# Kernel optimization log

Hardware: AMD Instinct MI355X
Metric: run time of the kernel (lower is better)

Reference implementation:

```python
import jax, jax.numpy as jnp
import numpy as np
from jax import lax

B, T, E, H, VC, VP = 128, 512, 256, 512, 64, 128


def _uniform(key, shape, bound):
    return jax.random.uniform(key, shape, minval=-bound, maxval=bound, dtype=jnp.float32)


def setup_inputs() -> dict:
    key = jax.random.key(0)
    ks = jax.random.split(key, 12)
    src = jax.random.randint(ks[0], (B, T), 0, VC)
    src_lengths = jax.random.randint(ks[1], (B,), 1, T + 1)
    # embedding table, padding_idx=0 row zeroed (as nn.Embedding does)
    emb_table = jax.random.normal(ks[2], (VC, E), dtype=jnp.float32)
    emb_table = emb_table.at[0].set(0.0)
    # layer 0: W_xh Linear(E->H, bias), W_hh Linear(H->H, no bias)
    bE, bH = 1.0 / np.sqrt(E), 1.0 / np.sqrt(H)
    W_xh0 = _uniform(ks[3], (E, H), bE)
    b_xh0 = _uniform(ks[4], (H,), bE)
    W_hh0 = _uniform(ks[5], (H, H), bH)
    # layer 1: input is hidden of layer 0
    W_xh1 = _uniform(ks[6], (H, H), bH)
    b_xh1 = _uniform(ks[7], (H,), bH)
    W_hh1 = _uniform(ks[8], (H, H), bH)
    # output projection Linear(H -> VP)
    fc_w = _uniform(ks[9], (H, VP), bH)
    fc_b = _uniform(ks[10], (VP,), bH)
    return {
        "src": src, "src_lengths": src_lengths, "emb_table": emb_table,
        "W_xh0": W_xh0, "b_xh0": b_xh0, "W_hh0": W_hh0,
        "W_xh1": W_xh1, "b_xh1": b_xh1, "W_hh1": W_hh1,
        "fc_w": fc_w, "fc_b": fc_b,
    }


def reference(src, src_lengths, emb_table, W_xh0, b_xh0, W_hh0,
              W_xh1, b_xh1, W_hh1, fc_w, fc_b):
    batch, seq_len = src.shape
    emb = emb_table[src]  # (B, T, E); dropout p=0 -> identity (eval)
    mask = jnp.arange(seq_len)[None, :] < src_lengths[:, None]  # (B, T) bool

    xs = jnp.transpose(emb, (1, 0, 2))          # (T, B, E) time-major
    ms = jnp.transpose(mask)[:, :, None]        # (T, B, 1)

    def step(h, inp):
        x_t, m_t = inp
        h0, h1 = h
        h0_new = jnp.tanh(x_t @ W_xh0 + b_xh0 + h0 @ W_hh0)
        h0 = jnp.where(m_t, h0_new, h0)
        h1_new = jnp.tanh(h0 @ W_xh1 + b_xh1 + h1 @ W_hh1)
        h1 = jnp.where(m_t, h1_new, h1)
        return (h0, h1), h1

    h_init = jnp.zeros((batch, W_hh0.shape[0]), dtype=emb.dtype)
    _, ys = lax.scan(step, (h_init, h_init), (xs, ms))  # ys: (T, B, H)
    outputs = jnp.transpose(ys, (1, 0, 2))               # (B, T, H)
    logits = outputs @ fc_w + fc_b                       # (B, T, VP)
    return logits
```

## Files before the change

### kernel.cpp

```cpp
#include <hip/hip_runtime.h>
#include <hip/hip_bf16.h>

constexpr int NB = 128;
constexpr int NT = 512;
constexpr int NE = 256;
constexpr int NH = 512;
constexpr int NV = 64;
constexpr int NP = 128;

constexpr int GROUPS = 8;
constexpr int MR     = 16;
constexpr int NCS    = 64;
constexpr int SLICES = 8;
constexpr int NBLK   = GROUPS * SLICES;
constexpr int RING   = 16;
constexpr int FS     = 32;

typedef unsigned short u16;
typedef __attribute__((ext_vector_type(8))) short bf16x8v;
typedef __attribute__((ext_vector_type(4))) float f32x4v;
typedef __attribute__((ext_vector_type(4))) unsigned u32x4;

__device__ __forceinline__ u16 f2bf(float x) {
  unsigned u = __builtin_bit_cast(unsigned, x);
  return (u16)((u + 0x7fffu + ((u >> 16) & 1u)) >> 16);
}

__device__ __forceinline__ void ld2_sc1_x4(const void* p0, const void* p1,
                                           u32x4& a, u32x4& b) {
  asm volatile("global_load_dwordx4 %0, %2, off sc1\n\t"
               "global_load_dwordx4 %1, %3, off sc1\n\t"
               "s_waitcnt vmcnt(0)"
               : "=&v"(a), "=&v"(b) : "v"(p0), "v"(p1) : "memory");
}
__device__ __forceinline__ void ld4_sc1_x4(const void* p0, const void* p1,
                                           const void* p2, const void* p3,
                                           u32x4& a, u32x4& b,
                                           u32x4& c, u32x4& d) {
  asm volatile("global_load_dwordx4 %0, %4, off sc1\n\t"
               "global_load_dwordx4 %1, %5, off sc1\n\t"
               "global_load_dwordx4 %2, %6, off sc1\n\t"
               "global_load_dwordx4 %3, %7, off sc1\n\t"
               "s_waitcnt vmcnt(0)"
               : "=&v"(a), "=&v"(b), "=&v"(c), "=&v"(d)
               : "v"(p0), "v"(p1), "v"(p2), "v"(p3) : "memory");
}
__device__ __forceinline__ void st_sc1_x4(void* p, u32x4 v) {
  asm volatile("global_store_dwordx4 %0, %1, off sc1" :: "v"(p), "v"(v) : "memory");
}

__global__ __launch_bounds__(256) void proj_kernel(
    const float* __restrict__ emb, const float* __restrict__ W_xh0,
    const float* __restrict__ b_xh0, float* __restrict__ proj) {
  int v = blockIdx.x >> 1;
  int j = ((blockIdx.x & 1) << 8) + threadIdx.x;
  float acc = b_xh0[j];
  const float* er = emb + v * NE;
  for (int e = 0; e < NE; ++e) acc += er[e] * W_xh0[e * NH + j];
  proj[v * NH + j] = acc;
}

__global__ __launch_bounds__(256) void transpose_bf16_kernel(
    const float* __restrict__ src, u16* __restrict__ dst, int R, int logC) {
  int idx = blockIdx.x * 256 + threadIdx.x;
  int C = 1 << logC;
  if (idx >= R * C) return;
  int r = idx >> logC;
  int c = idx & (C - 1);
  dst[c * R + r] = f2bf(src[idx]);
}

__global__ void zero_flags_kernel(int* flags) {
  int i = blockIdx.x * 256 + threadIdx.x;
  if (i < NBLK * FS) flags[i] = 0;
}

__device__ __forceinline__ bf16x8v frag_A(const u16* __restrict__ buf,
                                          int kt, int lane) {
  return *(const bf16x8v*)(buf + (kt << 9) + (((lane ^ kt) & 63) << 3));
}

__global__ __launch_bounds__(512, 1) void rnn_persist(
    const int* __restrict__ src, const int* __restrict__ lens,
    const float* __restrict__ proj,
    const u16* __restrict__ Wt_hh0,
    const u16* __restrict__ Wt_xh1,
    const u16* __restrict__ Wt_hh1,
    const float* __restrict__ b_xh1,
    u16* __restrict__ h0_ring,
    u16* __restrict__ h1_all,
    int* __restrict__ flags)
{
  __shared__ struct {
    u16 a0[16 * 512];
    u16 a1[16 * 512];
    float pj[NV][72];
    int srcv[MR][NT];
    u16 rep0[16][72];
    u16 rep1[16][72];
  } sm;

  const int bid = blockIdx.x;
  const int g = bid & (GROUPS - 1);
  const int slice = bid >> 3;
  const int c0 = slice * NCS;
  const int r0 = g * MR;

  const int tid = threadIdx.x;
  const int lane = tid & 63, wave = tid >> 6;
  const int lq = lane >> 4, lr = lane & 15;
  const bool l1w = (wave >= 4);
  const int n0 = (wave & 3) * 16;
  const size_t HS = (size_t)NB * NH;

  int* myflag = flags + bid * FS;

  bf16x8v w0[16], wx[16], wh[16];
  if (!l1w) {
    const u16* wp = Wt_hh0 + (size_t)(c0 + n0 + lr) * NH + lq * 8;
#pragma unroll
    for (int kt = 0; kt < 16; ++kt) w0[kt] = *(const bf16x8v*)(wp + kt * 32);
  } else {
    const u16* wpx = Wt_xh1 + (size_t)(c0 + n0 + lr) * NH + lq * 8;
    const u16* wph = Wt_hh1 + (size_t)(c0 + n0 + lr) * NH + lq * 8;
#pragma unroll
    for (int kt = 0; kt < 16; ++kt) {
      wx[kt] = *(const bf16x8v*)(wpx + kt * 32);
      wh[kt] = *(const bf16x8v*)(wph + kt * 32);
    }
  }
  const float bcol = l1w ? b_xh1[c0 + n0 + lr] : 0.f;

#pragma unroll
  for (int it = 0; it < 2; ++it) {
    int c = it * 512 + tid;
    int v = c >> 4, j4 = (c & 15) * 4;
    *(float4*)&sm.pj[v][j4] = *(const float4*)&proj[v * NH + c0 + j4];
  }
#pragma unroll
  for (int it = 0; it < 4; ++it)
    ((int4*)sm.srcv)[it * 512 + tid] =
        ((const int4*)(src + (size_t)r0 * NT))[it * 512 + tid];

  int ln[4];
#pragma unroll
  for (int i = 0; i < 4; ++i) ln[i] = lens[r0 + lq * 4 + i];
  u16 oreg[4] = {0, 0, 0, 0};
  __syncthreads();

  for (int s = 0; s <= NT; ++s) {
    if (s > 0) {
      if (tid < 8) {
        const int* fp = flags + (((tid * 8) | g)) * FS;
        while (__hip_atomic_load(fp, __ATOMIC_RELAXED,
                                 __HIP_MEMORY_SCOPE_AGENT) < s) {}
      }
      if (tid < 64) __builtin_amdgcn_fence(__ATOMIC_ACQUIRE, "agent");
      __syncthreads();
      {
        const u16* g0 = h0_ring + (size_t)((s - 1) & (RING - 1)) * HS +
                        (size_t)r0 * NH;
        int idx0 = tid, idx1 = 512 + tid;
        int row0 = idx0 >> 6, k80 = idx0 & 63;
        int row1 = idx1 >> 6, k81 = idx1 & 63;
        int kt0 = k80 >> 2, s0 = (((k80 & 3) << 4) | row0) ^ kt0;
        int kt1 = k81 >> 2, s1 = (((k81 & 3) << 4) | row1) ^ kt1;
        if (s >= 2) {
          const u16* g1 = h1_all + (size_t)(s - 2) * HS + (size_t)r0 * NH;
          u32x4 a, b, c, d;
          ld4_sc1_x4(g0 + row0 * NH + k80 * 8, g0 + row1 * NH + k81 * 8,
                     g1 + row0 * NH + k80 * 8, g1 + row1 * NH + k81 * 8,
                     a, b, c, d);
          *(u32x4*)(sm.a0 + (kt0 << 9) + (s0 << 3)) = a;
          *(u32x4*)(sm.a0 + (kt1 << 9) + (s1 << 3)) = b;
          *(u32x4*)(sm.a1 + (kt0 << 9) + (s0 << 3)) = c;
          *(u32x4*)(sm.a1 + (kt1 << 9) + (s1 << 3)) = d;
        } else {
          u32x4 a, b;
          ld2_sc1_x4(g0 + row0 * NH + k80 * 8, g0 + row1 * NH + k81 * 8, a, b);
          *(u32x4*)(sm.a0 + (kt0 << 9) + (s0 << 3)) = a;
          *(u32x4*)(sm.a0 + (kt1 << 9) + (s1 << 3)) = b;
        }
      }
      __syncthreads();
    }

    if (!l1w) {
      if (s < NT) {
        f32x4v acc = {0.f, 0.f, 0.f, 0.f};
        if (s > 0) {
#pragma unroll
          for (int kt = 0; kt < 16; ++kt)
            acc = __builtin_amdgcn_mfma_f32_16x16x32_bf16(
                frag_A(sm.a0, kt, lane), w0[kt], acc, 0, 0, 0);
        }
#pragma unroll
        for (int i = 0; i < 4; ++i) {
          int row = lq * 4 + i;
          float pre = acc[i] + sm.pj[sm.srcv[row][s]][n0 + lr];
          oreg[i] = (s < ln[i]) ? f2bf(tanhf(pre)) : oreg[i];
          sm.rep0[row][n0 + lr] = oreg[i];
        }
      }
    } else {
      if (s >= 1) {
        const int t = s - 1;
        f32x4v accx = {0.f, 0.f, 0.f, 0.f}, acch = {0.f, 0.f, 0.f, 0.f};
#pragma unroll
        for (int kt = 0; kt < 16; ++kt)
          accx = __builtin_amdgcn_mfma_f32_16x16x32_bf16(
              frag_A(sm.a0, kt, lane), wx[kt], accx, 0, 0, 0);
        if (s >= 2) {
#pragma unroll
          for (int kt = 0; kt < 16; ++kt)
            acch = __builtin_amdgcn_mfma_f32_16x16x32_bf16(
                frag_A(sm.a1, kt, lane), wh[kt], acch, 0, 0, 0);
        }
#pragma unroll
        for (int i = 0; i < 4; ++i) {
          int row = lq * 4 + i;
          float pre = accx[i] + acch[i] + bcol;
          oreg[i] = (t < ln[i]) ? f2bf(tanhf(pre)) : oreg[i];
          sm.rep1[row][n0 + lr] = oreg[i];
        }
      }
    }
    __syncthreads();

    if (tid < 256) {
      int p = tid >> 7, e = tid & 127;
      int row = e >> 3, q = e & 7;
      if (p == 0) {
        if (s < NT)
          st_sc1_x4(h0_ring + (size_t)(s & (RING - 1)) * HS +
                        (size_t)(r0 + row) * NH + c0 + q * 8,
                    *(const u32x4*)&sm.rep0[row][q * 8]);
      } else if (s >= 1) {
        st_sc1_x4(h1_all + (size_t)(s - 1) * HS +
                      (size_t)(r0 + row) * NH + c0 + q * 8,
                  *(const u32x4*)&sm.rep1[row][q * 8]);
      }
    }
    asm volatile("s_waitcnt vmcnt(0)" ::: "memory");
    __syncthreads();
    if (tid == 0)
      __hip_atomic_store(myflag, s + 1, __ATOMIC_RELAXED,
                         __HIP_MEMORY_SCOPE_AGENT);
  }
}

__global__ __launch_bounds__(256) void out_gemm(
    const u16* __restrict__ h1_all, const u16* __restrict__ fc_wT,
    const float* __restrict__ fc_b, float* __restrict__ out)
{
  const int t = blockIdx.x;
  const int tid = threadIdx.x, lane = tid & 63, wave = tid >> 6;
  const int lq = lane >> 4, lr = lane & 15;
  const int m0 = wave * 32;
  f32x4v acc[2][8];
#pragma unroll
  for (int a = 0; a < 2; ++a)
#pragma unroll
    for (int b = 0; b < 8; ++b) acc[a][b] = (f32x4v){0.f, 0.f, 0.f, 0.f};

  const u16* a0p = h1_all + ((size_t)t * NB + m0 + lr) * NH;
  const u16* a1p = a0p + 16 * NH;
#pragma unroll 2
  for (int kt = 0; kt < 16; ++kt) {
    int kb = kt * 32 + lq * 8;
    bf16x8v a0 = *(const bf16x8v*)(a0p + kb);
    bf16x8v a1 = *(const bf16x8v*)(a1p + kb);
#pragma unroll
    for (int ni = 0; ni < 8; ++ni) {
      bf16x8v bb = *(const bf16x8v*)(fc_wT + (size_t)(ni * 16 + lr) * NH + kb);
      acc[0][ni] = __builtin_amdgcn_mfma_f32_16x16x32_bf16(a0, bb, acc[0][ni], 0, 0, 0);
      acc[1][ni] = __builtin_amdgcn_mfma_f32_16x16x32_bf16(a1, bb, acc[1][ni], 0, 0, 0);
    }
  }
#pragma unroll
  for (int mi = 0; mi < 2; ++mi)
#pragma unroll
    for (int ni = 0; ni < 8; ++ni)
#pragma unroll
      for (int i = 0; i < 4; ++i) {
        int b_ = m0 + mi * 16 + lq * 4 + i;
        int p = ni * 16 + lr;
        out[((size_t)b_ * NT + t) * NP + p] = acc[mi][ni][i] + fc_b[p];
      }
}

extern "C" void kernel_launch(void* const* d_in, const int* in_sizes, int n_in,
                              void* d_out, int out_size, void* d_ws, size_t ws_size,
                              hipStream_t stream) {
  const int*   src   = (const int*)  d_in[0];
  const int*   lens  = (const int*)  d_in[1];
  const float* emb   = (const float*)d_in[2];
  const float* W_xh0 = (const float*)d_in[3];
  const float* b_xh0 = (const float*)d_in[4];
  const float* W_hh0 = (const float*)d_in[5];
  const float* W_xh1 = (const float*)d_in[6];
  const float* b_xh1 = (const float*)d_in[7];
  const float* W_hh1 = (const float*)d_in[8];
  const float* fc_w  = (const float*)d_in[9];
  const float* fc_b  = (const float*)d_in[10];
  float* out = (float*)d_out;

  char* ws = (char*)d_ws;
  auto alloc = [&](size_t bytes) { char* p = ws; ws += (bytes + 255) & ~size_t(255); return p; };
  float* proj   = (float*)alloc(NV * NH * 4);
  u16* Wt_hh0   = (u16*)  alloc(NH * NH * 2);
  u16* Wt_xh1   = (u16*)  alloc(NH * NH * 2);
  u16* Wt_hh1   = (u16*)  alloc(NH * NH * 2);
  u16* fc_wT    = (u16*)  alloc(NP * NH * 2);
  u16* h0_ring  = (u16*)  alloc((size_t)RING * NB * NH * 2);
  u16* h1_all   = (u16*)  alloc((size_t)NT * NB * NH * 2);
  int* flags    = (int*)  alloc(NBLK * FS * 4);

  proj_kernel<<<NV * 2, 256, 0, stream>>>(emb, W_xh0, b_xh0, proj);
  transpose_bf16_kernel<<<(NH * NH + 255) / 256, 256, 0, stream>>>(W_hh0, Wt_hh0, NH, 9);
  transpose_bf16_kernel<<<(NH * NH + 255) / 256, 256, 0, stream>>>(W_xh1, Wt_xh1, NH, 9);
  transpose_bf16_kernel<<<(NH * NH + 255) / 256, 256, 0, stream>>>(W_hh1, Wt_hh1, NH, 9);
  transpose_bf16_kernel<<<(NH * NP + 255) / 256, 256, 0, stream>>>(fc_w, fc_wT, NH, 7);
  zero_flags_kernel<<<(NBLK * FS + 255) / 256, 256, 0, stream>>>(flags);

  {
    void* kargs[] = { (void*)&src, (void*)&lens, (void*)&proj, (void*)&Wt_hh0,
                      (void*)&Wt_xh1, (void*)&Wt_hh1, (void*)&b_xh1,
                      (void*)&h0_ring, (void*)&h1_all, (void*)&flags };
    hipError_t e = hipLaunchCooperativeKernel((void*)rnn_persist, dim3(NBLK), dim3(512),
                                              kargs, 0, stream);
    if (e != hipSuccess) {
      rnn_persist<<<NBLK, 512, 0, stream>>>(src, lens, proj, Wt_hh0, Wt_xh1,
                                            Wt_hh1, b_xh1, h0_ring, h1_all, flags);
    }
  }

  out_gemm<<<NT, 256, 0, stream>>>(h1_all, fc_wT, fc_b, out);
}
```

Before: 1.833 ms.

## Split RNN layers into separate block sets with pre-swizzled fragment layout

Splits the persistent kernel so layer 0 and layer 1 run on separate 256-thread blocks (128 blocks total) with their own flag arrays. Layer 0 can now run up to RING-2 steps ahead of layer 1 instead of advancing in lockstep. Hidden states are published in an MFMA-fragment-swizzled panel layout, so loads copy straight into LDS without per-element index math, and out_gemm reads that layout directly. The cost is twice as many blocks needing co-residency and more cross-block flag polling.

Result: faster. 1.547 ms (-15.6%).

```diff
diff --git a/kernel.cpp b/kernel.cpp
--- a/kernel.cpp
+++ b/kernel.cpp
@@ -12,7 +12,7 @@
 constexpr int MR     = 16;
 constexpr int NCS    = 64;
 constexpr int SLICES = 8;
-constexpr int NBLK   = GROUPS * SLICES;
+constexpr int NBLK   = GROUPS * SLICES * 2;
 constexpr int RING   = 16;
 constexpr int FS     = 32;
 
@@ -26,17 +26,9 @@
   return (u16)((u + 0x7fffu + ((u >> 16) & 1u)) >> 16);
 }
 
-__device__ __forceinline__ void ld2_sc1_x4(const void* p0, const void* p1,
-                                           u32x4& a, u32x4& b) {
-  asm volatile("global_load_dwordx4 %0, %2, off sc1\n\t"
-               "global_load_dwordx4 %1, %3, off sc1\n\t"
-               "s_waitcnt vmcnt(0)"
-               : "=&v"(a), "=&v"(b) : "v"(p0), "v"(p1) : "memory");
-}
-__device__ __forceinline__ void ld4_sc1_x4(const void* p0, const void* p1,
-                                           const void* p2, const void* p3,
-                                           u32x4& a, u32x4& b,
-                                           u32x4& c, u32x4& d) {
+__device__ __forceinline__ void ld4_sc1(const void* p0, const void* p1,
+                                        const void* p2, const void* p3,
+                                        u32x4& a, u32x4& b, u32x4& c, u32x4& d) {
   asm volatile("global_load_dwordx4 %0, %4, off sc1\n\t"
                "global_load_dwordx4 %1, %5, off sc1\n\t"
                "global_load_dwordx4 %2, %6, off sc1\n\t"
@@ -44,6 +36,26 @@
                "s_waitcnt vmcnt(0)"
                : "=&v"(a), "=&v"(b), "=&v"(c), "=&v"(d)
                : "v"(p0), "v"(p1), "v"(p2), "v"(p3) : "memory");
+}
+__device__ __forceinline__ void ld8_sc1(const void* p0, const void* p1,
+                                        const void* p2, const void* p3,
+                                        const void* p4, const void* p5,
+                                        const void* p6, const void* p7,
+                                        u32x4& a, u32x4& b, u32x4& c, u32x4& d,
+                                        u32x4& e, u32x4& f, u32x4& g, u32x4& h) {
+  asm volatile("global_load_dwordx4 %0, %8, off sc1\n\t"
+               "global_load_dwordx4 %1, %9, off sc1\n\t"
+               "global_load_dwordx4 %2, %10, off sc1\n\t"
+               "global_load_dwordx4 %3, %11, off sc1\n\t"
+               "global_load_dwordx4 %4, %12, off sc1\n\t"
+               "global_load_dwordx4 %5, %13, off sc1\n\t"
+               "global_load_dwordx4 %6, %14, off sc1\n\t"
+               "global_load_dwordx4 %7, %15, off sc1\n\t"
+               "s_waitcnt vmcnt(0)"
+               : "=&v"(a), "=&v"(b), "=&v"(c), "=&v"(d),
+                 "=&v"(e), "=&v"(f), "=&v"(g), "=&v"(h)
+               : "v"(p0), "v"(p1), "v"(p2), "v"(p3),
+                 "v"(p4), "v"(p5), "v"(p6), "v"(p7) : "memory");
 }
 __device__ __forceinline__ void st_sc1_x4(void* p, u32x4 v) {
   asm volatile("global_store_dwordx4 %0, %1, off sc1" :: "v"(p), "v"(v) : "memory");
@@ -72,7 +84,7 @@
 
 __global__ void zero_flags_kernel(int* flags) {
   int i = blockIdx.x * 256 + threadIdx.x;
-  if (i < NBLK * FS) flags[i] = 0;
+  if (i < 2 * 64 * FS) flags[i] = 0;
 }
 
 __device__ __forceinline__ bf16x8v frag_A(const u16* __restrict__ buf,
@@ -80,177 +92,218 @@
   return *(const bf16x8v*)(buf + (kt << 9) + (((lane ^ kt) & 63) << 3));
 }
 
-__global__ __launch_bounds__(512, 1) void rnn_persist(
+__device__ __forceinline__ void publish_slice(const u16* __restrict__ rep,
+                                              u16* __restrict__ gpanel,
+                                              int sl, int tid) {
+  if (tid < 128) {
+    int ktl = tid >> 6, slot = tid & 63;
+    int ktp = sl * 2 + ktl;
+    int v = (slot ^ ktp) & 63;
+    int row = v & 15, koct = (v >> 4) & 3;
+    int lcol = ktl * 32 + koct * 8;
+    st_sc1_x4(gpanel + ktp * 512 + slot * 8,
+              *(const u32x4*)(rep + row * 64 + lcol));
+  }
+}
+
+__global__ __launch_bounds__(256, 1) void rnn_persist(
     const int* __restrict__ src, const int* __restrict__ lens,
     const float* __restrict__ proj,
     const u16* __restrict__ Wt_hh0,
     const u16* __restrict__ Wt_xh1,
     const u16* __restrict__ Wt_hh1,
     const float* __restrict__ b_xh1,
-    u16* __restrict__ h0_ring,
-    u16* __restrict__ h1_all,
+    u16* __restrict__ h0f,
+    u16* __restrict__ h1f,
     int* __restrict__ flags)
 {
   __shared__ struct {
-    u16 a0[16 * 512];
-    u16 a1[16 * 512];
-    float pj[NV][72];
-    int srcv[MR][NT];
-    u16 rep0[16][72];
-    u16 rep1[16][72];
+    union {
+      struct { __attribute__((aligned(16))) u16 a0[8192];
+               float pj[NV][68]; int srcv[MR][NT]; } l0;
+      struct { __attribute__((aligned(16))) u16 a0[8192];
+               __attribute__((aligned(16))) u16 a1[8192]; } l1;
+    } u;
+    __attribute__((aligned(16))) u16 rep[16][64];
   } sm;
 
   const int bid = blockIdx.x;
-  const int g = bid & (GROUPS - 1);
-  const int slice = bid >> 3;
-  const int c0 = slice * NCS;
+  const bool is_l1 = (bid >= 64);
+  const int rb = bid & 63;
+  const int g = rb & (GROUPS - 1);
+  const int sl = rb >> 3;
+  const int c0 = sl * NCS;
   const int r0 = g * MR;
 
   const int tid = threadIdx.x;
   const int lane = tid & 63, wave = tid >> 6;
   const int lq = lane >> 4, lr = lane & 15;
-  const bool l1w = (wave >= 4);
-  const int n0 = (wave & 3) * 16;
-  const size_t HS = (size_t)NB * NH;
-
-  int* myflag = flags + bid * FS;
-
-  bf16x8v w0[16], wx[16], wh[16];
-  if (!l1w) {
-    const u16* wp = Wt_hh0 + (size_t)(c0 + n0 + lr) * NH + lq * 8;
-#pragma unroll
-    for (int kt = 0; kt < 16; ++kt) w0[kt] = *(const bf16x8v*)(wp + kt * 32);
-  } else {
-    const u16* wpx = Wt_xh1 + (size_t)(c0 + n0 + lr) * NH + lq * 8;
-    const u16* wph = Wt_hh1 + (size_t)(c0 + n0 + lr) * NH + lq * 8;
-#pragma unroll
-    for (int kt = 0; kt < 16; ++kt) {
-      wx[kt] = *(const bf16x8v*)(wpx + kt * 32);
-      wh[kt] = *(const bf16x8v*)(wph + kt * 32);
-    }
-  }
-  const float bcol = l1w ? b_xh1[c0 + n0 + lr] : 0.f;
-
-#pragma unroll
-  for (int it = 0; it < 2; ++it) {
-    int c = it * 512 + tid;
-    int v = c >> 4, j4 = (c & 15) * 4;
-    *(float4*)&sm.pj[v][j4] = *(const float4*)&proj[v * NH + c0 + j4];
-  }
-#pragma unroll
-  for (int it = 0; it < 4; ++it)
-    ((int4*)sm.srcv)[it * 512 + tid] =
-        ((const int4*)(src + (size_t)r0 * NT))[it * 512 + tid];
+  const int lcol = wave * 16 + lr;
+
+  int* flag0 = flags;
+  int* flag1 = flags + 64 * FS;
+  int* myflag = (is_l1 ? flag1 : flag0) + rb * FS;
 
   int ln[4];
 #pragma unroll
   for (int i = 0; i < 4; ++i) ln[i] = lens[r0 + lq * 4 + i];
   u16 oreg[4] = {0, 0, 0, 0};
-  __syncthreads();
-
-  for (int s = 0; s <= NT; ++s) {
-    if (s > 0) {
+
+  if (!is_l1) {
+    bf16x8v w0[16];
+    {
+      const u16* wp = Wt_hh0 + (size_t)(c0 + lcol) * NH + lq * 8;
+#pragma unroll
+      for (int kt = 0; kt < 16; ++kt) w0[kt] = *(const bf16x8v*)(wp + kt * 32);
+    }
+#pragma unroll
+    for (int it = 0; it < 4; ++it) {
+      int c = it * 256 + tid;
+      int v = c >> 4, j4 = (c & 15) * 4;
+      *(float4*)&sm.u.l0.pj[v][j4] = *(const float4*)&proj[v * NH + c0 + j4];
+    }
+#pragma unroll
+    for (int it = 0; it < 8; ++it)
+      ((int4*)sm.u.l0.srcv)[it * 256 + tid] =
+          ((const int4*)(src + (size_t)r0 * NT))[it * 256 + tid];
+    __syncthreads();
+
+    for (int s = 0; s < NT; ++s) {
+      f32x4v acc = {0.f, 0.f, 0.f, 0.f};
+      if (s > 0) {
+        if (tid < 8) {
+          const int* fp = flag0 + ((tid * 8) | g) * FS;
+          while (__hip_atomic_load(fp, __ATOMIC_RELAXED,
+                                   __HIP_MEMORY_SCOPE_AGENT) < s) {}
+        } else if (tid < 16 && s - 14 > 0) {
+          const int* fp = flag1 + (((tid - 8) * 8) | g) * FS;
+          while (__hip_atomic_load(fp, __ATOMIC_RELAXED,
+                                   __HIP_MEMORY_SCOPE_AGENT) < s - 14) {}
+        }
+        if (tid < 64) __builtin_amdgcn_fence(__ATOMIC_ACQUIRE, "agent");
+        __syncthreads();
+        {
+          const u16* gp = h0f + ((size_t)((s - 1) & (RING - 1)) * GROUPS + g) * 8192;
+          u32x4 a, b, c, d;
+          ld4_sc1(gp + (tid + 0) * 8, gp + (tid + 256) * 8,
+                  gp + (tid + 512) * 8, gp + (tid + 768) * 8, a, b, c, d);
+          *(u32x4*)(sm.u.l0.a0 + (tid + 0) * 8) = a;
+          *(u32x4*)(sm.u.l0.a0 + (tid + 256) * 8) = b;
+          *(u32x4*)(sm.u.l0.a0 + (tid + 512) * 8) = c;
+          *(u32x4*)(sm.u.l0.a0 + (tid + 768) * 8) = d;
+        }
+        __syncthreads();
+#pragma unroll
+        for (int kt = 0; kt < 16; ++kt)
+          acc = __builtin_amdgcn_mfma_f32_16x16x32_bf16(
+              frag_A(sm.u.l0.a0, kt, lane), w0[kt], acc, 0, 0, 0);
+      }
+#pragma unroll
+      for (int i = 0; i < 4; ++i) {
+        int row = lq * 4 + i;
+        float pre = acc[i] + sm.u.l0.pj[sm.u.l0.srcv[row][s]][lcol];
+        oreg[i] = (s < ln[i]) ? f2bf(tanhf(pre)) : oreg[i];
+        sm.rep[row][lcol] = oreg[i];
+      }
+      __syncthreads();
+      publish_slice(&sm.rep[0][0],
+                    h0f + ((size_t)(s & (RING - 1)) * GROUPS + g) * 8192, sl, tid);
+      asm volatile("s_waitcnt vmcnt(0)" ::: "memory");
+      __syncthreads();
+      if (tid == 0)
+        __hip_atomic_store(myflag, s + 1, __ATOMIC_RELAXED,
+                           __HIP_MEMORY_SCOPE_AGENT);
+    }
+  } else {
+    bf16x8v wx[16], wh[16];
+    {
+      const u16* wpx = Wt_xh1 + (size_t)(c0 + lcol) * NH + lq * 8;
+      const u16* wph = Wt_hh1 + (size_t)(c0 + lcol) * NH + lq * 8;
+#pragma unroll
+      for (int kt = 0; kt < 16; ++kt) {
+        wx[kt] = *(const bf16x8v*)(wpx + kt * 32);
+        wh[kt] = *(const bf16x8v*)(wph + kt * 32);
+      }
+    }
+    const float bcol = b_xh1[c0 + lcol];
+    __syncthreads();
+
+    for (int t = 0; t < NT; ++t) {
       if (tid < 8) {
-        const int* fp = flags + (((tid * 8) | g)) * FS;
+        if (t > 0) {
+          const int* fp = flag1 + ((tid * 8) | g) * FS;
+          while (__hip_atomic_load(fp, __ATOMIC_RELAXED,
+                                   __HIP_MEMORY_SCOPE_AGENT) < t) {}
+        }
+      } else if (tid < 16) {
+        const int* fp = flag0 + (((tid - 8) * 8) | g) * FS;
         while (__hip_atomic_load(fp, __ATOMIC_RELAXED,
-                                 __HIP_MEMORY_SCOPE_AGENT) < s) {}
+                                 __HIP_MEMORY_SCOPE_AGENT) < t + 1) {}
       }
       if (tid < 64) __builtin_amdgcn_fence(__ATOMIC_ACQUIRE, "agent");
       __syncthreads();
       {
-        const u16* g0 = h0_ring + (size_t)((s - 1) & (RING - 1)) * HS +
-                        (size_t)r0 * NH;
-        int idx0 = tid, idx1 = 512 + tid;
-        int row0 = idx0 >> 6, k80 = idx0 & 63;
-        int row1 = idx1 >> 6, k81 = idx1 & 63;
-        int kt0 = k80 >> 2, s0 = (((k80 & 3) << 4) | row0) ^ kt0;
-        int kt1 = k81 >> 2, s1 = (((k81 & 3) << 4) | row1) ^ kt1;
-        if (s >= 2) {
-          const u16* g1 = h1_all + (size_t)(s - 2) * HS + (size_t)r0 * NH;
+        const u16* g0 = h0f + ((size_t)(t & (RING - 1)) * GROUPS + g) * 8192;
+        if (t > 0) {
+          const u16* g1 = h1f + ((size_t)(t - 1) * GROUPS + g) * 8192;
+          u32x4 a, b, c, d, e, f, h, k;
+          ld8_sc1(g0 + (tid + 0) * 8, g0 + (tid + 256) * 8,
+                  g0 + (tid + 512) * 8, g0 + (tid + 768) * 8,
+                  g1 + (tid + 0) * 8, g1 + (tid + 256) * 8,
+                  g1 + (tid + 512) * 8, g1 + (tid + 768) * 8,
+                  a, b, c, d, e, f, h, k);
+          *(u32x4*)(sm.u.l1.a0 + (tid + 0) * 8) = a;
+          *(u32x4*)(sm.u.l1.a0 + (tid + 256) * 8) = b;
+          *(u32x4*)(sm.u.l1.a0 + (tid + 512) * 8) = c;
+          *(u32x4*)(sm.u.l1.a0 + (tid + 768) * 8) = d;
+          *(u32x4*)(sm.u.l1.a1 + (tid + 0) * 8) = e;
+          *(u32x4*)(sm.u.l1.a1 + (tid + 256) * 8) = f;
+          *(u32x4*)(sm.u.l1.a1 + (tid + 512) * 8) = h;
+          *(u32x4*)(sm.u.l1.a1 + (tid + 768) * 8) = k;
+        } else {
           u32x4 a, b, c, d;
-          ld4_sc1_x4(g0 + row0 * NH + k80 * 8, g0 + row1 * NH + k81 * 8,
-                     g1 + row0 * NH + k80 * 8, g1 + row1 * NH + k81 * 8,
-                     a, b, c, d);
-          *(u32x4*)(sm.a0 + (kt0 << 9) + (s0 << 3)) = a;
-          *(u32x4*)(sm.a0 + (kt1 << 9) + (s1 << 3)) = b;
-          *(u32x4*)(sm.a1 + (kt0 << 9) + (s0 << 3)) = c;
-          *(u32x4*)(sm.a1 + (kt1 << 9) + (s1 << 3)) = d;
-        } else {
-          u32x4 a, b;
-          ld2_sc1_x4(g0 + row0 * NH + k80 * 8, g0 + row1 * NH + k81 * 8, a, b);
-          *(u32x4*)(sm.a0 + (kt0 << 9) + (s0 << 3)) = a;
-          *(u32x4*)(sm.a0 + (kt1 << 9) + (s1 << 3)) = b;
+          ld4_sc1(g0 + (tid + 0) * 8, g0 + (tid + 256) * 8,
+                  g0 + (tid + 512) * 8, g0 + (tid + 768) * 8, a, b, c, d);
+          *(u32x4*)(sm.u.l1.a0 + (tid + 0) * 8) = a;
+          *(u32x4*)(sm.u.l1.a0 + (tid + 256) * 8) = b;
+          *(u32x4*)(sm.u.l1.a0 + (tid + 512) * 8) = c;
+          *(u32x4*)(sm.u.l1.a0 + (tid + 768) * 8) = d;
         }
       }
       __syncthreads();
-    }
-
-    if (!l1w) {
-      if (s < NT) {
-        f32x4v acc = {0.f, 0.f, 0.f, 0.f};
-        if (s > 0) {
-#pragma unroll
-          for (int kt = 0; kt < 16; ++kt)
-            acc = __builtin_amdgcn_mfma_f32_16x16x32_bf16(
-                frag_A(sm.a0, kt, lane), w0[kt], acc, 0, 0, 0);
-        }
-#pragma unroll
-        for (int i = 0; i < 4; ++i) {
-          int row = lq * 4 + i;
-          float pre = acc[i] + sm.pj[sm.srcv[row][s]][n0 + lr];
-          oreg[i] = (s < ln[i]) ? f2bf(tanhf(pre)) : oreg[i];
-          sm.rep0[row][n0 + lr] = oreg[i];
-        }
-      }
-    } else {
-      if (s >= 1) {
-        const int t = s - 1;
-        f32x4v accx = {0.f, 0.f, 0.f, 0.f}, acch = {0.f, 0.f, 0.f, 0.f};
+
+      f32x4v accx = {0.f, 0.f, 0.f, 0.f}, acch = {0.f, 0.f, 0.f, 0.f};
+#pragma unroll
+      for (int kt = 0; kt < 16; ++kt)
+        accx = __builtin_amdgcn_mfma_f32_16x16x32_bf16(
+            frag_A(sm.u.l1.a0, kt, lane), wx[kt], accx, 0, 0, 0);
+      if (t > 0) {
 #pragma unroll
         for (int kt = 0; kt < 16; ++kt)
-          accx = __builtin_amdgcn_mfma_f32_16x16x32_bf16(
-              frag_A(sm.a0, kt, lane), wx[kt], accx, 0, 0, 0);
-        if (s >= 2) {
-#pragma unroll
-          for (int kt = 0; kt < 16; ++kt)
-            acch = __builtin_amdgcn_mfma_f32_16x16x32_bf16(
-                frag_A(sm.a1, kt, lane), wh[kt], acch, 0, 0, 0);
-        }
-#pragma unroll
-        for (int i = 0; i < 4; ++i) {
-          int row = lq * 4 + i;
-          float pre = accx[i] + acch[i] + bcol;
-          oreg[i] = (t < ln[i]) ? f2bf(tanhf(pre)) : oreg[i];
-          sm.rep1[row][n0 + lr] = oreg[i];
-        }
-      }
-    }
-    __syncthreads();
-
-    if (tid < 256) {
-      int p = tid >> 7, e = tid & 127;
-      int row = e >> 3, q = e & 7;
-      if (p == 0) {
-        if (s < NT)
-          st_sc1_x4(h0_ring + (size_t)(s & (RING - 1)) * HS +
-                        (size_t)(r0 + row) * NH + c0 + q * 8,
-                    *(const u32x4*)&sm.rep0[row][q * 8]);
-      } else if (s >= 1) {
-        st_sc1_x4(h1_all + (size_t)(s - 1) * HS +
-                      (size_t)(r0 + row) * NH + c0 + q * 8,
-                  *(const u32x4*)&sm.rep1[row][q * 8]);
-      }
-    }
-    asm volatile("s_waitcnt vmcnt(0)" ::: "memory");
-    __syncthreads();
-    if (tid == 0)
-      __hip_atomic_store(myflag, s + 1, __ATOMIC_RELAXED,
-                         __HIP_MEMORY_SCOPE_AGENT);
+          acch = __builtin_amdgcn_mfma_f32_16x16x32_bf16(
+              frag_A(sm.u.l1.a1, kt, lane), wh[kt], acch, 0, 0, 0);
+      }
+#pragma unroll
+      for (int i = 0; i < 4; ++i) {
+        int row = lq * 4 + i;
+        float pre = accx[i] + acch[i] + bcol;
+        oreg[i] = (t < ln[i]) ? f2bf(tanhf(pre)) : oreg[i];
+        sm.rep[row][lcol] = oreg[i];
+      }
+      __syncthreads();
+      publish_slice(&sm.rep[0][0],
+                    h1f + ((size_t)t * GROUPS + g) * 8192, sl, tid);
+      asm volatile("s_waitcnt vmcnt(0)" ::: "memory");
+      __syncthreads();
+      if (tid == 0)
+        __hip_atomic_store(myflag, t + 1, __ATOMIC_RELAXED,
+                           __HIP_MEMORY_SCOPE_AGENT);
+    }
   }
 }
 
 __global__ __launch_bounds__(256) void out_gemm(
-    const u16* __restrict__ h1_all, const u16* __restrict__ fc_wT,
+    const u16* __restrict__ h1f, const u16* __restrict__ fc_wT,
     const float* __restrict__ fc_b, float* __restrict__ out)
 {
   const int t = blockIdx.x;
@@ -263,13 +316,13 @@
 #pragma unroll
     for (int b = 0; b < 8; ++b) acc[a][b] = (f32x4v){0.f, 0.f, 0.f, 0.f};
 
-  const u16* a0p = h1_all + ((size_t)t * NB + m0 + lr) * NH;
-  const u16* a1p = a0p + 16 * NH;
+  const u16* p0 = h1f + ((size_t)t * GROUPS + wave * 2) * 8192;
+  const u16* p1 = p0 + 8192;
 #pragma unroll 2
   for (int kt = 0; kt < 16; ++kt) {
+    bf16x8v a0 = *(const bf16x8v*)(p0 + kt * 512 + (((lane ^ kt) & 63) << 3));
+    bf16x8v a1 = *(const bf16x8v*)(p1 + kt * 512 + (((lane ^ kt) & 63) << 3));
     int kb = kt * 32 + lq * 8;
-    bf16x8v a0 = *(const bf16x8v*)(a0p + kb);
-    bf16x8v a1 = *(const bf16x8v*)(a1p + kb);
 #pragma unroll
     for (int ni = 0; ni < 8; ++ni) {
       bf16x8v bb = *(const bf16x8v*)(fc_wT + (size_t)(ni * 16 + lr) * NH + kb);
@@ -312,28 +365,28 @@
   u16* Wt_xh1   = (u16*)  alloc(NH * NH * 2);
   u16* Wt_hh1   = (u16*)  alloc(NH * NH * 2);
   u16* fc_wT    = (u16*)  alloc(NP * NH * 2);
-  u16* h0_ring  = (u16*)  alloc((size_t)RING * NB * NH * 2);
-  u16* h1_all   = (u16*)  alloc((size_t)NT * NB * NH * 2);
-  int* flags    = (int*)  alloc(NBLK * FS * 4);
+  u16* h0f      = (u16*)  alloc((size_t)RING * GROUPS * 8192 * 2);
+  u16* h1f      = (u16*)  alloc((size_t)NT * GROUPS * 8192 * 2);
+  int* flags    = (int*)  alloc(2 * 64 * FS * 4);
 
   proj_kernel<<<NV * 2, 256, 0, stream>>>(emb, W_xh0, b_xh0, proj);
   transpose_bf16_kernel<<<(NH * NH + 255) / 256, 256, 0, stream>>>(W_hh0, Wt_hh0, NH, 9);
   transpose_bf16_kernel<<<(NH * NH + 255) / 256, 256, 0, stream>>>(W_xh1, Wt_xh1, NH, 9);
   transpose_bf16_kernel<<<(NH * NH + 255) / 256, 256, 0, stream>>>(W_hh1, Wt_hh1, NH, 9);
   transpose_bf16_kernel<<<(NH * NP + 255) / 256, 256, 0, stream>>>(fc_w, fc_wT, NH, 7);
-  zero_flags_kernel<<<(NBLK * FS + 255) / 256, 256, 0, stream>>>(flags);
+  zero_flags_kernel<<<(2 * 64 * FS + 255) / 256, 256, 0, stream>>>(flags);
 
   {
     void* kargs[] = { (void*)&src, (void*)&lens, (void*)&proj, (void*)&Wt_hh0,
                       (void*)&Wt_xh1, (void*)&Wt_hh1, (void*)&b_xh1,
-                      (void*)&h0_ring, (void*)&h1_all, (void*)&flags };
-    hipError_t e = hipLaunchCooperativeKernel((void*)rnn_persist, dim3(NBLK), dim3(512),
+                      (void*)&h0f, (void*)&h1f, (void*)&flags };
+    hipError_t e = hipLaunchCooperativeKernel((void*)rnn_persist, dim3(NBLK), dim3(256),
                                               kargs, 0, stream);
     if (e != hipSuccess) {
-      rnn_persist<<<NBLK, 512, 0, stream>>>(src, lens, proj, Wt_hh0, Wt_xh1,
-                                            Wt_hh1, b_xh1, h0_ring, h1_all, flags);
+      rnn_persist<<<NBLK, 256, 0, stream>>>(src, lens, proj, Wt_hh0, Wt_xh1,
+                                            Wt_hh1, b_xh1, h0f, h1f, flags);
     }
   }
 
-  out_gemm<<<NT, 256, 0, stream>>>(h1_all, fc_wT, fc_b, out);
-}
+  out_gemm<<<NT, 256, 0, stream>>>(h1f, fc_wT, fc_b, out);
+}
```
